# Optimization experiments

Hardware: AMD Instinct MI355X
Metric: run time of the kernel (lower is better)

## Reference

```python
import jax, jax.numpy as jnp
import numpy as np

N, P, D = 262144, 128, 64
EPS = 1e-5
NEG = -1e30


def setup_inputs() -> dict:
    key = jax.random.key(0)
    ks = jax.random.split(key, 12)
    feature = jax.random.normal(ks[0], (N, D), jnp.float32)
    feature_geo = jax.random.normal(ks[1], (N, D), jnp.float32)
    xyz = jax.random.uniform(ks[2], (N, 3), jnp.float32)
    centers = jax.random.uniform(ks[3], (3,), jnp.float32)
    plane_center = jax.random.uniform(ks[4], (P, 3), jnp.float32)
    nrm = jax.random.normal(ks[5], (P, 3), jnp.float32)
    plane_normal = nrm / jnp.linalg.norm(nrm, axis=1, keepdims=True)
    lo = 0.3 * jax.random.uniform(ks[6], (P, 3), jnp.float32)
    hi = 0.5 + 0.5 * jax.random.uniform(ks[7], (P, 3), jnp.float32)
    # exactly two active axes per plane (one axis of the aabb is zeroed)
    ax = jnp.arange(P) % 3
    keep = (jnp.arange(3)[None, :] != ax[:, None]).astype(jnp.float32)
    plane_xyz_min = lo * keep
    plane_xyz_max = hi * keep
    w1 = 0.05 * jax.random.normal(ks[8], (2 * D, D), jnp.float32)
    b1 = jnp.zeros((D,), jnp.float32)
    w2 = 0.05 * jax.random.normal(ks[9], (D, D), jnp.float32)
    b2 = jnp.zeros((D,), jnp.float32)
    w3 = 0.05 * jax.random.normal(ks[10], (D, 1), jnp.float32)
    b3 = jnp.zeros((1,), jnp.float32)
    g1 = jnp.ones((D,), jnp.float32); be1 = jnp.zeros((D,), jnp.float32)
    m1 = jnp.zeros((D,), jnp.float32); v1 = jnp.ones((D,), jnp.float32)
    g2 = jnp.ones((D,), jnp.float32); be2 = jnp.zeros((D,), jnp.float32)
    m2 = jnp.zeros((D,), jnp.float32); v2 = jnp.ones((D,), jnp.float32)
    return dict(feature=feature, feature_geo=feature_geo, xyz=xyz, centers=centers,
                plane_center=plane_center, plane_normal=plane_normal,
                plane_xyz_min=plane_xyz_min, plane_xyz_max=plane_xyz_max,
                w1=w1, b1=b1, g1=g1, be1=be1, m1=m1, v1=v1,
                w2=w2, b2=b2, g2=g2, be2=be2, m2=m2, v2=v2,
                w3=w3, b3=b3)


def _bn(x, g, b, m, v):
    return (x - m) * (g * jax.lax.rsqrt(v + EPS)) + b


def reference(feature, feature_geo, xyz, centers, plane_center, plane_normal,
              plane_xyz_min, plane_xyz_max, w1, b1, g1, be1, m1, v1,
              w2, b2, g2, be2, m2, v2, w3, b3):
    clouds = xyz + centers                                   # [N,3]
    f = jnp.concatenate([feature, feature_geo], axis=1)      # [N,2D]
    # 1x1 conv MLP == per-point matmul (fc1 -> fc2 with BN+ReLU, fc3)
    h1 = jax.nn.relu(_bn(f @ w1 + b1, g1, be1, m1, v1))      # [N,D]
    h2 = jax.nn.relu(_bn(h1 @ w2 + b2, g2, be2, m2, v2))     # [N,D]
    scores = jax.nn.relu(h2 @ w3 + b3)[:, 0]                 # [N]
    # per-plane aabb mask over the two active axes (xyz_max != 0)
    active = plane_xyz_max != 0                              # [P,3]
    in_rng = (clouds[None] >= plane_xyz_min[:, None]) & (clouds[None] < plane_xyz_max[:, None])
    range_mask = jnp.all(in_rng | ~active[:, None, :], axis=-1)   # [P,N]
    # point-to-plane distance: |(clouds - center) . normal|
    dots = clouds @ plane_normal.T                           # [N,P]
    offs = jnp.sum(plane_center * plane_normal, axis=1)      # [P]
    dist = jnp.abs(dots - offs[None, :]).T                   # [P,N]
    mask = range_mask & (dist < 0.1)                         # [P,N]
    sig = jax.nn.sigmoid(scores)                             # [N]
    on_mask = mask & (sig > 0.5)[None, :]
    off_mask = mask & (sig <= 0.5)[None, :]

    def pool(m):  # masked max-pool of fc2 features over points of one plane
        val = jnp.max(jnp.where(m[:, None], h2, NEG), axis=0)     # [D]
        return jnp.where(jnp.any(m), val, 0.0)

    on_feat = jax.lax.map(pool, on_mask)                     # [P,D]
    off_feat = jax.lax.map(pool, off_mask)                   # [P,D]
    scores_masked = jnp.where(mask, scores[None, :], 0.0)    # [P,N]
    return scores_masked, mask, on_mask, off_mask, on_feat, off_feat
```

## Files before the change

kernel.cpp:

```cpp
#include <hip/hip_runtime.h>
#include <hip/hip_bf16.h>
#include <math.h>

#define NPTS 262144
#define NP   128
#define DD   64
#define NWORDS (NPTS / 64)

#define AS4 __attribute__((address_space(4)))
typedef float evf4 __attribute__((ext_vector_type(4)));
typedef AS4 const float* csf;
typedef AS4 const evf4*  csf4;
#define TO_CSF(p)  ((csf)(unsigned long long)(const void*)(p))
#define TO_CSF4(p) ((csf4)(unsigned long long)(const void*)(p))

__global__ __launch_bounds__(256) void prep_kernel(
    const float* __restrict__ plane_center, const float* __restrict__ plane_normal,
    const float* __restrict__ pmin, const float* __restrict__ pmax,
    const float* __restrict__ w2,
    float* __restrict__ packed, float* __restrict__ w2T,
    float* __restrict__ out_feats)
{
    const int t = threadIdx.x;
    out_feats[blockIdx.x * 256 + t] = 0.0f;
    if (blockIdx.x == 0 && t < NP) {
        float n0 = plane_normal[t*3+0], n1 = plane_normal[t*3+1], n2 = plane_normal[t*3+2];
        float c0 = plane_center[t*3+0], c1 = plane_center[t*3+1], c2 = plane_center[t*3+2];
        float off = (c0*n0 + c1*n1) + c2*n2;
        float4* pp = reinterpret_cast<float4*>(packed) + t * 3;
        pp[0] = make_float4(n0, n1, n2, off);
        pp[1] = make_float4(pmin[t*3+0], pmin[t*3+1], pmin[t*3+2], 0.0f);
        pp[2] = make_float4(pmax[t*3+0], pmax[t*3+1], pmax[t*3+2], 0.0f);
    }
    if (blockIdx.x == 1) {
#pragma unroll
        for (int u = 0; u < 16; ++u) {
            const int e = u * 256 + t;
            const int j = e >> 6, k = e & 63;
            w2T[e] = w2[k * DD + j];
        }
    }
}

__global__ __launch_bounds__(256) void fused_kernel(
    const float* __restrict__ feature, const float* __restrict__ feature_geo,
    const float* __restrict__ xyz, const float* __restrict__ centers,
    const float* __restrict__ packed,
    const float* __restrict__ w1, const float* __restrict__ b1,
    const float* __restrict__ g1, const float* __restrict__ be1,
    const float* __restrict__ m1, const float* __restrict__ v1,
    const float* __restrict__ w2T, const float* __restrict__ b2,
    const float* __restrict__ g2, const float* __restrict__ be2,
    const float* __restrict__ m2, const float* __restrict__ v2,
    const float* __restrict__ w3, const float* __restrict__ b3,
    float* __restrict__ h2_out,
    float* __restrict__ out_sm, float* __restrict__ out_mask,
    float* __restrict__ out_on, float* __restrict__ out_off,
    unsigned long long* __restrict__ hitOn, unsigned long long* __restrict__ hitOff)
{
    const int t = threadIdx.x;
    const int n = blockIdx.x * 256 + t;
    const int lane = t & 63;
    const int word = n >> 6;

    const csf  cc  = TO_CSF(centers);
    const csf4 pp  = TO_CSF4(packed);
    const csf  w1c = TO_CSF(w1);

    const float c0 = xyz[n*3+0] + cc[0];
    const float c1 = xyz[n*3+1] + cc[1];
    const float c2 = xyz[n*3+2] + cc[2];

    unsigned long long mklo = 0ull, mkhi = 0ull;

    float acc[DD];
#pragma unroll
    for (int j = 0; j < DD; ++j) acc[j] = 0.0f;

    const float4* fA = reinterpret_cast<const float4*>(feature) + (size_t)n * 16;
    const float4* fB = reinterpret_cast<const float4*>(feature_geo) + (size_t)n * 16;
#pragma unroll 1
    for (int q = 0; q < 16; ++q) {
        const float4 fv = fA[q];
        const csf wr = w1c + q * 4 * DD;
#pragma unroll
        for (int j = 0; j < DD; ++j) acc[j] = fmaf(fv.x, wr[j], acc[j]);
#pragma unroll
        for (int j = 0; j < DD; ++j) acc[j] = fmaf(fv.y, wr[DD + j], acc[j]);
#pragma unroll
        for (int j = 0; j < DD; ++j) acc[j] = fmaf(fv.z, wr[2 * DD + j], acc[j]);
#pragma unroll
        for (int j = 0; j < DD; ++j) acc[j] = fmaf(fv.w, wr[3 * DD + j], acc[j]);
#pragma unroll
        for (int u = 0; u < 4; ++u) {
            const int p = q * 4 + u;
            const evf4 nrm = pp[p*3+0];
            const evf4 mn  = pp[p*3+1];
            const evf4 mx  = pp[p*3+2];
            float d = fabsf(fmaf(c2, nrm.z, fmaf(c1, nrm.y, c0 * nrm.x)) - nrm.w);
            bool ok0 = (mx.x == 0.0f) | ((c0 >= mn.x) & (c0 < mx.x));
            bool ok1 = (mx.y == 0.0f) | ((c1 >= mn.y) & (c1 < mx.y));
            bool ok2 = (mx.z == 0.0f) | ((c2 >= mn.z) & (c2 < mx.z));
            bool mk  = ok0 & ok1 & ok2 & (d < 0.1f);
            __builtin_nontemporal_store(mk ? 1.0f : 0.0f, &out_mask[(size_t)p * NPTS + n]);
            mklo |= ((unsigned long long)mk) << p;
        }
    }
    const csf w1b = w1c + DD * DD;
#pragma unroll 1
    for (int q = 0; q < 16; ++q) {
        const float4 fv = fB[q];
        const csf wr = w1b + q * 4 * DD;
#pragma unroll
        for (int j = 0; j < DD; ++j) acc[j] = fmaf(fv.x, wr[j], acc[j]);
#pragma unroll
        for (int j = 0; j < DD; ++j) acc[j] = fmaf(fv.y, wr[DD + j], acc[j]);
#pragma unroll
        for (int j = 0; j < DD; ++j) acc[j] = fmaf(fv.z, wr[2 * DD + j], acc[j]);
#pragma unroll
        for (int j = 0; j < DD; ++j) acc[j] = fmaf(fv.w, wr[3 * DD + j], acc[j]);
#pragma unroll
        for (int u = 0; u < 4; ++u) {
            const int p = 64 + q * 4 + u;
            const evf4 nrm = pp[p*3+0];
            const evf4 mn  = pp[p*3+1];
            const evf4 mx  = pp[p*3+2];
            float d = fabsf(fmaf(c2, nrm.z, fmaf(c1, nrm.y, c0 * nrm.x)) - nrm.w);
            bool ok0 = (mx.x == 0.0f) | ((c0 >= mn.x) & (c0 < mx.x));
            bool ok1 = (mx.y == 0.0f) | ((c1 >= mn.y) & (c1 < mx.y));
            bool ok2 = (mx.z == 0.0f) | ((c2 >= mn.z) & (c2 < mx.z));
            bool mk  = ok0 & ok1 & ok2 & (d < 0.1f);
            __builtin_nontemporal_store(mk ? 1.0f : 0.0f, &out_mask[(size_t)p * NPTS + n]);
            mkhi |= ((unsigned long long)mk) << (p - 64);
        }
    }
    {
        const csf g1c = TO_CSF(g1), v1c = TO_CSF(v1), b1c = TO_CSF(b1),
                  m1c = TO_CSF(m1), be1c = TO_CSF(be1);
#pragma unroll
        for (int j = 0; j < DD; ++j) {
            float sc = g1c[j] * (1.0f / sqrtf(v1c[j] + 1e-5f));
            float h  = fmaf(acc[j] + b1c[j] - m1c[j], sc, be1c[j]);
            acc[j] = fmaxf(h, 0.0f);
        }
    }

    const csf w2t = TO_CSF(w2T);
    const csf g2c = TO_CSF(g2), v2c = TO_CSF(v2), b2c = TO_CSF(b2),
              m2c = TO_CSF(m2), be2c = TO_CSF(be2), w3c = TO_CSF(w3);
    float s = 0.0f;
    float4* o = reinterpret_cast<float4*>(h2_out) + (size_t)n * 16;
#pragma unroll 1
    for (int jq = 0; jq < 16; ++jq) {
        const csf r0 = w2t + (4*jq + 0) * DD;
        const csf r1 = w2t + (4*jq + 1) * DD;
        const csf r2 = w2t + (4*jq + 2) * DD;
        const csf r3 = w2t + (4*jq + 3) * DD;
        float a0 = 0.0f, a1 = 0.0f, a2 = 0.0f, a3 = 0.0f;
#pragma unroll
        for (int k = 0; k < DD; ++k) {
            const float h = acc[k];
            a0 = fmaf(h, r0[k], a0);
            a1 = fmaf(h, r1[k], a1);
            a2 = fmaf(h, r2[k], a2);
            a3 = fmaf(h, r3[k], a3);
        }
        float hv[4] = {a0, a1, a2, a3};
#pragma unroll
        for (int u = 0; u < 4; ++u) {
            const int jj = 4*jq + u;
            float sc = g2c[jj] * (1.0f / sqrtf(v2c[jj] + 1e-5f));
            float h  = fmaf(hv[u] + b2c[jj] - m2c[jj], sc, be2c[jj]);
            h = fmaxf(h, 0.0f);
            hv[u] = h;
            s = fmaf(h, w3c[jj], s);
        }
        o[jq] = make_float4(hv[0], hv[1], hv[2], hv[3]);
    }
    s += TO_CSF(b3)[0];
    const float score = fmaxf(s, 0.0f);

    const bool on = (0.5f + 0.5f * tanhf(0.5f * score)) > 0.5f;

#pragma unroll 1
    for (int p = 0; p < 64; ++p) {
        const bool mk = (mklo >> p) & 1ull;
        const size_t idx = (size_t)p * NPTS + n;
        const bool mon  = mk & on;
        const bool moff = mk & (!on);
        __builtin_nontemporal_store(mk ? score : 0.0f, &out_sm[idx]);
        __builtin_nontemporal_store(mon ? 1.0f : 0.0f, &out_on[idx]);
        __builtin_nontemporal_store(moff ? 1.0f : 0.0f, &out_off[idx]);
        unsigned long long bOn  = __ballot(mon);
        unsigned long long bOff = __ballot(moff);
        if (lane == 0) {
            hitOn [(size_t)p * NWORDS + word] = bOn;
            hitOff[(size_t)p * NWORDS + word] = bOff;
        }
    }
#pragma unroll 1
    for (int p = 64; p < 128; ++p) {
        const bool mk = (mkhi >> (p - 64)) & 1ull;
        const size_t idx = (size_t)p * NPTS + n;
        const bool mon  = mk & on;
        const bool moff = mk & (!on);
        __builtin_nontemporal_store(mk ? score : 0.0f, &out_sm[idx]);
        __builtin_nontemporal_store(mon ? 1.0f : 0.0f, &out_on[idx]);
        __builtin_nontemporal_store(moff ? 1.0f : 0.0f, &out_off[idx]);
        unsigned long long bOn  = __ballot(mon);
        unsigned long long bOff = __ballot(moff);
        if (lane == 0) {
            hitOn [(size_t)p * NWORDS + word] = bOn;
            hitOff[(size_t)p * NWORDS + word] = bOff;
        }
    }
}

__global__ __launch_bounds__(256) void pool_kernel(
    const float* __restrict__ h2,
    const unsigned long long* __restrict__ hitOn,
    const unsigned long long* __restrict__ hitOff,
    int* __restrict__ out_feats_i)
{
    __shared__ float tile[128 * DD];
    __shared__ unsigned long long bm[2][NP][2];
    const int t = threadIdx.x;
    const int lane = t & 63;
    const int wv = t >> 6;

    float accOn[32], accOff[32];
#pragma unroll
    for (int i = 0; i < 32; ++i) { accOn[i] = 0.0f; accOff[i] = 0.0f; }

    for (int cc = 0; cc < 4; ++cc) {
        const int chunk = blockIdx.x * 4 + cc;
        const int base  = chunk * 128;
        const float4* src = reinterpret_cast<const float4*>(h2 + (size_t)base * DD);
        float4* dst = reinterpret_cast<float4*>(tile);
#pragma unroll
        for (int q = 0; q < 8; ++q) dst[t + q * 256] = src[t + q * 256];
        {
            const int p = t & 127;
            const int half = t >> 7;
            const unsigned long long* hsrc = half ? hitOff : hitOn;
            const int w0 = chunk * 2;
            bm[half][p][0] = hsrc[(size_t)p * NWORDS + w0 + 0];
            bm[half][p][1] = hsrc[(size_t)p * NWORDS + w0 + 1];
        }
        __syncthreads();

#pragma unroll
        for (int i = 0; i < 32; ++i) {
            const int p = wv * 32 + i;
            unsigned long long m;
            m = bm[0][p][0];
            while (m) { int nn = __builtin_ctzll(m); m &= m - 1;
                        accOn[i]  = fmaxf(accOn[i],  tile[nn * DD + lane]); }
            m = bm[0][p][1];
            while (m) { int nn = __builtin_ctzll(m); m &= m - 1;
                        accOn[i]  = fmaxf(accOn[i],  tile[(64 + nn) * DD + lane]); }
            m = bm[1][p][0];
            while (m) { int nn = __builtin_ctzll(m); m &= m - 1;
                        accOff[i] = fmaxf(accOff[i], tile[nn * DD + lane]); }
            m = bm[1][p][1];
            while (m) { int nn = __builtin_ctzll(m); m &= m - 1;
                        accOff[i] = fmaxf(accOff[i], tile[(64 + nn) * DD + lane]); }
        }
        __syncthreads();
    }
#pragma unroll
    for (int i = 0; i < 32; ++i) {
        const int p = wv * 32 + i;
        if (accOn[i]  != 0.0f) atomicMax(&out_feats_i[p * DD + lane],            __float_as_int(accOn[i]));
        if (accOff[i] != 0.0f) atomicMax(&out_feats_i[NP * DD + p * DD + lane],  __float_as_int(accOff[i]));
    }
}

extern "C" void kernel_launch(void* const* d_in, const int* in_sizes, int n_in,
                              void* d_out, int out_size, void* d_ws, size_t ws_size,
                              hipStream_t stream) {
    const float* feature      = (const float*)d_in[0];
    const float* feature_geo  = (const float*)d_in[1];
    const float* xyz          = (const float*)d_in[2];
    const float* centers      = (const float*)d_in[3];
    const float* plane_center = (const float*)d_in[4];
    const float* plane_normal = (const float*)d_in[5];
    const float* pmin         = (const float*)d_in[6];
    const float* pmax         = (const float*)d_in[7];
    const float* w1 = (const float*)d_in[8];
    const float* b1 = (const float*)d_in[9];
    const float* g1 = (const float*)d_in[10];
    const float* be1 = (const float*)d_in[11];
    const float* m1 = (const float*)d_in[12];
    const float* v1 = (const float*)d_in[13];
    const float* w2 = (const float*)d_in[14];
    const float* b2 = (const float*)d_in[15];
    const float* g2 = (const float*)d_in[16];
    const float* be2 = (const float*)d_in[17];
    const float* m2 = (const float*)d_in[18];
    const float* v2 = (const float*)d_in[19];
    const float* w3 = (const float*)d_in[20];
    const float* b3 = (const float*)d_in[21];

    float* out = (float*)d_out;
    const size_t PN = (size_t)NP * NPTS;
    float* out_sm    = out;
    float* out_mask  = out + PN;
    float* out_on    = out + 2 * PN;
    float* out_off   = out + 3 * PN;
    float* out_feats = out + 4 * PN;

    float* h2     = (float*)d_ws;
    unsigned long long* hitOn  = (unsigned long long*)(h2 + (size_t)NPTS * DD);
    unsigned long long* hitOff = hitOn + (size_t)NP * NWORDS;
    float* packed = (float*)(hitOff + (size_t)NP * NWORDS);
    float* w2T    = packed + NP * 12;

    prep_kernel<<<64, 256, 0, stream>>>(
        plane_center, plane_normal, pmin, pmax, w2, packed, w2T, out_feats);
    fused_kernel<<<NPTS / 256, 256, 0, stream>>>(
        feature, feature_geo, xyz, centers, packed,
        w1, b1, g1, be1, m1, v1, w2T, b2, g2, be2, m2, v2, w3, b3,
        h2, out_sm, out_mask, out_on, out_off, hitOn, hitOff);
    pool_kernel<<<512, 256, 0, stream>>>(h2, hitOn, hitOff, (int*)out_feats);
}
```

Baseline: 850.7 us.

## Stage MLP weights in LDS and move mask computation into store loop

```diff
diff --git a/kernel.cpp b/kernel.cpp
--- a/kernel.cpp
+++ b/kernel.cpp
@@ -58,20 +58,30 @@
     float* __restrict__ out_on, float* __restrict__ out_off,
     unsigned long long* __restrict__ hitOn, unsigned long long* __restrict__ hitOff)
 {
+    __shared__ float sw1[128 * DD];
+    __shared__ float sw2[DD * DD];
     const int t = threadIdx.x;
     const int n = blockIdx.x * 256 + t;
     const int lane = t & 63;
     const int word = n >> 6;
 
-    const csf  cc  = TO_CSF(centers);
-    const csf4 pp  = TO_CSF4(packed);
-    const csf  w1c = TO_CSF(w1);
-
+    {
+        const float4* s1 = reinterpret_cast<const float4*>(w1);
+        const float4* s2 = reinterpret_cast<const float4*>(w2T);
+        float4* d1 = reinterpret_cast<float4*>(sw1);
+        float4* d2 = reinterpret_cast<float4*>(sw2);
+#pragma unroll
+        for (int k = 0; k < 8; ++k) d1[t + k * 256] = s1[t + k * 256];
+#pragma unroll
+        for (int k = 0; k < 4; ++k) d2[t + k * 256] = s2[t + k * 256];
+    }
+
+    const csf cc = TO_CSF(centers);
     const float c0 = xyz[n*3+0] + cc[0];
     const float c1 = xyz[n*3+1] + cc[1];
     const float c2 = xyz[n*3+2] + cc[2];
 
-    unsigned long long mklo = 0ull, mkhi = 0ull;
+    __syncthreads();
 
     float acc[DD];
 #pragma unroll
@@ -82,57 +92,60 @@
 #pragma unroll 1
     for (int q = 0; q < 16; ++q) {
         const float4 fv = fA[q];
-        const csf wr = w1c + q * 4 * DD;
-#pragma unroll
-        for (int j = 0; j < DD; ++j) acc[j] = fmaf(fv.x, wr[j], acc[j]);
-#pragma unroll
-        for (int j = 0; j < DD; ++j) acc[j] = fmaf(fv.y, wr[DD + j], acc[j]);
-#pragma unroll
-        for (int j = 0; j < DD; ++j) acc[j] = fmaf(fv.z, wr[2 * DD + j], acc[j]);
-#pragma unroll
-        for (int j = 0; j < DD; ++j) acc[j] = fmaf(fv.w, wr[3 * DD + j], acc[j]);
-#pragma unroll
-        for (int u = 0; u < 4; ++u) {
-            const int p = q * 4 + u;
-            const evf4 nrm = pp[p*3+0];
-            const evf4 mn  = pp[p*3+1];
-            const evf4 mx  = pp[p*3+2];
-            float d = fabsf(fmaf(c2, nrm.z, fmaf(c1, nrm.y, c0 * nrm.x)) - nrm.w);
-            bool ok0 = (mx.x == 0.0f) | ((c0 >= mn.x) & (c0 < mx.x));
-            bool ok1 = (mx.y == 0.0f) | ((c1 >= mn.y) & (c1 < mx.y));
-            bool ok2 = (mx.z == 0.0f) | ((c2 >= mn.z) & (c2 < mx.z));
-            bool mk  = ok0 & ok1 & ok2 & (d < 0.1f);
-            __builtin_nontemporal_store(mk ? 1.0f : 0.0f, &out_mask[(size_t)p * NPTS + n]);
-            mklo |= ((unsigned long long)mk) << p;
-        }
-    }
-    const csf w1b = w1c + DD * DD;
+        const evf4* wr = reinterpret_cast<const evf4*>(sw1 + q * 4 * DD);
+#pragma unroll
+        for (int j4 = 0; j4 < 16; ++j4) { const evf4 w = wr[j4];
+            acc[4*j4+0] = fmaf(fv.x, w.x, acc[4*j4+0]);
+            acc[4*j4+1] = fmaf(fv.x, w.y, acc[4*j4+1]);
+            acc[4*j4+2] = fmaf(fv.x, w.z, acc[4*j4+2]);
+            acc[4*j4+3] = fmaf(fv.x, w.w, acc[4*j4+3]); }
+#pragma unroll
+        for (int j4 = 0; j4 < 16; ++j4) { const evf4 w = wr[16 + j4];
+            acc[4*j4+0] = fmaf(fv.y, w.x, acc[4*j4+0]);
+            acc[4*j4+1] = fmaf(fv.y, w.y, acc[4*j4+1]);
+            acc[4*j4+2] = fmaf(fv.y, w.z, acc[4*j4+2]);
+            acc[4*j4+3] = fmaf(fv.y, w.w, acc[4*j4+3]); }
+#pragma unroll
+        for (int j4 = 0; j4 < 16; ++j4) { const evf4 w = wr[32 + j4];
+            acc[4*j4+0] = fmaf(fv.z, w.x, acc[4*j4+0]);
+            acc[4*j4+1] = fmaf(fv.z, w.y, acc[4*j4+1]);
+            acc[4*j4+2] = fmaf(fv.z, w.z, acc[4*j4+2]);
+            acc[4*j4+3] = fmaf(fv.z, w.w, acc[4*j4+3]); }
+#pragma unroll
+        for (int j4 = 0; j4 < 16; ++j4) { const evf4 w = wr[48 + j4];
+            acc[4*j4+0] = fmaf(fv.w, w.x, acc[4*j4+0]);
+            acc[4*j4+1] = fmaf(fv.w, w.y, acc[4*j4+1]);
+            acc[4*j4+2] = fmaf(fv.w, w.z, acc[4*j4+2]);
+            acc[4*j4+3] = fmaf(fv.w, w.w, acc[4*j4+3]); }
+    }
 #pragma unroll 1
     for (int q = 0; q < 16; ++q) {
         const float4 fv = fB[q];
-        const csf wr = w1b + q * 4 * DD;
-#pragma unroll
-        for (int j = 0; j < DD; ++j) acc[j] = fmaf(fv.x, wr[j], acc[j]);
-#pragma unroll
-        for (int j = 0; j < DD; ++j) acc[j] = fmaf(fv.y, wr[DD + j], acc[j]);
-#pragma unroll
-        for (int j = 0; j < DD; ++j) acc[j] = fmaf(fv.z, wr[2 * DD + j], acc[j]);
-#pragma unroll
-        for (int j = 0; j < DD; ++j) acc[j] = fmaf(fv.w, wr[3 * DD + j], acc[j]);
-#pragma unroll
-        for (int u = 0; u < 4; ++u) {
-            const int p = 64 + q * 4 + u;
-            const evf4 nrm = pp[p*3+0];
-            const evf4 mn  = pp[p*3+1];
-            const evf4 mx  = pp[p*3+2];
-            float d = fabsf(fmaf(c2, nrm.z, fmaf(c1, nrm.y, c0 * nrm.x)) - nrm.w);
-            bool ok0 = (mx.x == 0.0f) | ((c0 >= mn.x) & (c0 < mx.x));
-            bool ok1 = (mx.y == 0.0f) | ((c1 >= mn.y) & (c1 < mx.y));
-            bool ok2 = (mx.z == 0.0f) | ((c2 >= mn.z) & (c2 < mx.z));
-            bool mk  = ok0 & ok1 & ok2 & (d < 0.1f);
-            __builtin_nontemporal_store(mk ? 1.0f : 0.0f, &out_mask[(size_t)p * NPTS + n]);
-            mkhi |= ((unsigned long long)mk) << (p - 64);
-        }
+        const evf4* wr = reinterpret_cast<const evf4*>(sw1 + (DD + q * 4) * DD);
+#pragma unroll
+        for (int j4 = 0; j4 < 16; ++j4) { const evf4 w = wr[j4];
+            acc[4*j4+0] = fmaf(fv.x, w.x, acc[4*j4+0]);
+            acc[4*j4+1] = fmaf(fv.x, w.y, acc[4*j4+1]);
+            acc[4*j4+2] = fmaf(fv.x, w.z, acc[4*j4+2]);
+            acc[4*j4+3] = fmaf(fv.x, w.w, acc[4*j4+3]); }
+#pragma unroll
+        for (int j4 = 0; j4 < 16; ++j4) { const evf4 w = wr[16 + j4];
+            acc[4*j4+0] = fmaf(fv.y, w.x, acc[4*j4+0]);
+            acc[4*j4+1] = fmaf(fv.y, w.y, acc[4*j4+1]);
+            acc[4*j4+2] = fmaf(fv.y, w.z, acc[4*j4+2]);
+            acc[4*j4+3] = fmaf(fv.y, w.w, acc[4*j4+3]); }
+#pragma unroll
+        for (int j4 = 0; j4 < 16; ++j4) { const evf4 w = wr[32 + j4];
+            acc[4*j4+0] = fmaf(fv.z, w.x, acc[4*j4+0]);
+            acc[4*j4+1] = fmaf(fv.z, w.y, acc[4*j4+1]);
+            acc[4*j4+2] = fmaf(fv.z, w.z, acc[4*j4+2]);
+            acc[4*j4+3] = fmaf(fv.z, w.w, acc[4*j4+3]); }
+#pragma unroll
+        for (int j4 = 0; j4 < 16; ++j4) { const evf4 w = wr[48 + j4];
+            acc[4*j4+0] = fmaf(fv.w, w.x, acc[4*j4+0]);
+            acc[4*j4+1] = fmaf(fv.w, w.y, acc[4*j4+1]);
+            acc[4*j4+2] = fmaf(fv.w, w.z, acc[4*j4+2]);
+            acc[4*j4+3] = fmaf(fv.w, w.w, acc[4*j4+3]); }
     }
     {
         const csf g1c = TO_CSF(g1), v1c = TO_CSF(v1), b1c = TO_CSF(b1),
@@ -145,25 +158,30 @@
         }
     }
 
-    const csf w2t = TO_CSF(w2T);
     const csf g2c = TO_CSF(g2), v2c = TO_CSF(v2), b2c = TO_CSF(b2),
               m2c = TO_CSF(m2), be2c = TO_CSF(be2), w3c = TO_CSF(w3);
     float s = 0.0f;
     float4* o = reinterpret_cast<float4*>(h2_out) + (size_t)n * 16;
 #pragma unroll 1
     for (int jq = 0; jq < 16; ++jq) {
-        const csf r0 = w2t + (4*jq + 0) * DD;
-        const csf r1 = w2t + (4*jq + 1) * DD;
-        const csf r2 = w2t + (4*jq + 2) * DD;
-        const csf r3 = w2t + (4*jq + 3) * DD;
+        const evf4* r0 = reinterpret_cast<const evf4*>(sw2 + (4*jq + 0) * DD);
+        const evf4* r1 = reinterpret_cast<const evf4*>(sw2 + (4*jq + 1) * DD);
+        const evf4* r2 = reinterpret_cast<const evf4*>(sw2 + (4*jq + 2) * DD);
+        const evf4* r3 = reinterpret_cast<const evf4*>(sw2 + (4*jq + 3) * DD);
         float a0 = 0.0f, a1 = 0.0f, a2 = 0.0f, a3 = 0.0f;
 #pragma unroll
-        for (int k = 0; k < DD; ++k) {
-            const float h = acc[k];
-            a0 = fmaf(h, r0[k], a0);
-            a1 = fmaf(h, r1[k], a1);
-            a2 = fmaf(h, r2[k], a2);
-            a3 = fmaf(h, r3[k], a3);
+        for (int k4 = 0; k4 < 16; ++k4) {
+            const evf4 w0 = r0[k4], w1v = r1[k4], w2v = r2[k4], w3v = r3[k4];
+            const float h0 = acc[4*k4+0], h1v = acc[4*k4+1],
+                        h2v = acc[4*k4+2], h3v = acc[4*k4+3];
+            a0 = fmaf(h0, w0.x, a0); a0 = fmaf(h1v, w0.y, a0);
+            a0 = fmaf(h2v, w0.z, a0); a0 = fmaf(h3v, w0.w, a0);
+            a1 = fmaf(h0, w1v.x, a1); a1 = fmaf(h1v, w1v.y, a1);
+            a1 = fmaf(h2v, w1v.z, a1); a1 = fmaf(h3v, w1v.w, a1);
+            a2 = fmaf(h0, w2v.x, a2); a2 = fmaf(h1v, w2v.y, a2);
+            a2 = fmaf(h2v, w2v.z, a2); a2 = fmaf(h3v, w2v.w, a2);
+            a3 = fmaf(h0, w3v.x, a3); a3 = fmaf(h1v, w3v.y, a3);
+            a3 = fmaf(h2v, w3v.z, a3); a3 = fmaf(h3v, w3v.w, a3);
         }
         float hv[4] = {a0, a1, a2, a3};
 #pragma unroll
@@ -182,31 +200,24 @@
 
     const bool on = (0.5f + 0.5f * tanhf(0.5f * score)) > 0.5f;
 
+    const csf4 pp = TO_CSF4(packed);
 #pragma unroll 1
-    for (int p = 0; p < 64; ++p) {
-        const bool mk = (mklo >> p) & 1ull;
+    for (int p = 0; p < NP; ++p) {
+        const evf4 nrm = pp[p*3+0];
+        const evf4 mn  = pp[p*3+1];
+        const evf4 mx  = pp[p*3+2];
+        float d = fabsf(fmaf(c2, nrm.z, fmaf(c1, nrm.y, c0 * nrm.x)) - nrm.w);
+        bool ok0 = (mx.x == 0.0f) | ((c0 >= mn.x) & (c0 < mx.x));
+        bool ok1 = (mx.y == 0.0f) | ((c1 >= mn.y) & (c1 < mx.y));
+        bool ok2 = (mx.z == 0.0f) | ((c2 >= mn.z) & (c2 < mx.z));
+        bool mk  = ok0 & ok1 & ok2 & (d < 0.1f);
         const size_t idx = (size_t)p * NPTS + n;
         const bool mon  = mk & on;
         const bool moff = mk & (!on);
-        __builtin_nontemporal_store(mk ? score : 0.0f, &out_sm[idx]);
-        __builtin_nontemporal_store(mon ? 1.0f : 0.0f, &out_on[idx]);
-        __builtin_nontemporal_store(moff ? 1.0f : 0.0f, &out_off[idx]);
-        unsigned long long bOn  = __ballot(mon);
-        unsigned long long bOff = __ballot(moff);
-        if (lane == 0) {
-            hitOn [(size_t)p * NWORDS + word] = bOn;
-            hitOff[(size_t)p * NWORDS + word] = bOff;
-        }
-    }
-#pragma unroll 1
-    for (int p = 64; p < 128; ++p) {
-        const bool mk = (mkhi >> (p - 64)) & 1ull;
-        const size_t idx = (size_t)p * NPTS + n;
-        const bool mon  = mk & on;
-        const bool moff = mk & (!on);
-        __builtin_nontemporal_store(mk ? score : 0.0f, &out_sm[idx]);
-        __builtin_nontemporal_store(mon ? 1.0f : 0.0f, &out_on[idx]);
-        __builtin_nontemporal_store(moff ? 1.0f : 0.0f, &out_off[idx]);
+        out_mask[idx] = mk ? 1.0f : 0.0f;
+        out_sm[idx]   = mk ? score : 0.0f;
+        out_on[idx]   = mon ? 1.0f : 0.0f;
+        out_off[idx]  = moff ? 1.0f : 0.0f;
         unsigned long long bOn  = __ballot(mon);
         unsigned long long bOff = __ballot(moff);
         if (lane == 0) {
```

After: 835.8 us. Within noise of the previous version (-1.8%).
